# Optimization experiments

Hardware: AMD Instinct MI355X
Metric: run time of the kernel (lower is better)

Reference implementation:

```python
import jax, jax.numpy as jnp
import numpy as np

DIM, WIDTH, POOL, BATCH, SEQ = 4096, 4, 512, 256, 16

def setup_inputs() -> dict:
    key = jax.random.key(0)
    k1, k2, k3, k4 = jax.random.split(key, 4)
    x = jax.random.normal(k1, (BATCH, SEQ, DIM), dtype=jnp.float32)
    conv_state = jax.random.normal(k2, (POOL, WIDTH - 1, DIM), dtype=jnp.float32)
    weight = jax.random.normal(k3, (WIDTH, DIM), dtype=jnp.float32)
    bias = jax.random.normal(k4, (DIM,), dtype=jnp.float32)
    conv_state_indices = jnp.arange(BATCH, dtype=jnp.int32)
    return {"x": x, "conv_state": conv_state, "weight": weight,
            "bias": bias, "conv_state_indices": conv_state_indices}

def reference(x, conv_state, weight, bias, conv_state_indices):
    # x: [b, s, d]; conv_state: [pool, width-1, d]; weight: [width, d]
    b, s, d = x.shape
    width = weight.shape[0]
    state = conv_state[conv_state_indices]            # gather: [b, width-1, d]
    x_new = jnp.concatenate([state, x], axis=1)       # [b, width-1+s, d]
    # depthwise causal conv, width taps (small fixed loop over taps)
    out = bias
    for k in range(width):
        out = out + x_new[:, k:k + s, :] * weight[k]  # [b, s, d]
    out = jax.nn.silu(out)                            # activation=True
    new_state = x_new[:, -(width - 1):, :]            # [b, width-1, d]
    updated_conv_state = conv_state.at[conv_state_indices].set(new_state)
    return out, updated_conv_state
```

## Files before the change

### kernel.cpp

```cpp
#include <hip/hip_runtime.h>

constexpr int DIM   = 4096;
constexpr int WIDTH = 4;
constexpr int POOL  = 512;
constexpr int BATCH = 256;
constexpr int SEQ   = 16;

constexpr int D4_CHUNKS   = DIM / (4 * 256);
constexpr int CONV_BLOCKS = D4_CHUNKS * BATCH;

typedef float f32x4 __attribute__((ext_vector_type(4)));

__device__ __forceinline__ f32x4 ld4(const float* p) {
    return *reinterpret_cast<const f32x4*>(p);
}
__device__ __forceinline__ void st4(float* p, f32x4 v) {
    *reinterpret_cast<f32x4*>(p) = v;
}
__device__ __forceinline__ float fast_silu(float v) {
    return v * __builtin_amdgcn_rcpf(1.0f + __expf(-v));
}

__global__ __launch_bounds__(256, 4) void fused_conv_update_kernel(
    const float* __restrict__ x,
    const float* __restrict__ conv_state,
    const float* __restrict__ weight,
    const float* __restrict__ bias,
    const int*   __restrict__ idxs,
    float*       __restrict__ out,
    float*       __restrict__ out_state)
{
    const int blk   = blockIdx.x;
    const int b     = blk >> 2;
    const int chunk = blk & (D4_CHUNKS - 1);
    const int d     = (chunk * 256 + threadIdx.x) * 4;
    const int idx   = idxs[b];

    const float* xb = x + (size_t)b * SEQ * DIM + d;
    const float* st = conv_state + (size_t)idx * (WIDTH - 1) * DIM + d;

    f32x4 xv[SEQ + WIDTH - 1];
    xv[0] = ld4(st + 0 * DIM);
    xv[1] = ld4(st + 1 * DIM);
    xv[2] = ld4(st + 2 * DIM);
#pragma unroll
    for (int s = 0; s < SEQ; ++s)
        xv[WIDTH - 1 + s] = ld4(xb + (size_t)s * DIM);

    const f32x4 w0 = ld4(weight + 0 * DIM + d);
    const f32x4 w1 = ld4(weight + 1 * DIM + d);
    const f32x4 w2 = ld4(weight + 2 * DIM + d);
    const f32x4 w3 = ld4(weight + 3 * DIM + d);
    const f32x4 bs = ld4(bias + d);

    __builtin_amdgcn_sched_barrier(0);

    float* ob = out + (size_t)b * SEQ * DIM + d;
#pragma unroll
    for (int s = 0; s < SEQ; ++s) {
        f32x4 acc = bs + xv[s] * w0 + xv[s + 1] * w1 + xv[s + 2] * w2 + xv[s + 3] * w3;
        acc.x = fast_silu(acc.x);
        acc.y = fast_silu(acc.y);
        acc.z = fast_silu(acc.z);
        acc.w = fast_silu(acc.w);
        st4(ob + (size_t)s * DIM, acc);
    }

    float* sd = out_state + (size_t)idx * (WIDTH - 1) * DIM + d;
    st4(sd + 0 * DIM, xv[SEQ + 0]);
    st4(sd + 1 * DIM, xv[SEQ + 1]);
    st4(sd + 2 * DIM, xv[SEQ + 2]);

    const int row     = blk >> 1;
    const int halfsel = blk & 1;

    __shared__ int skip;
    if (threadIdx.x == 0) skip = 0;
    __syncthreads();
    if (idxs[threadIdx.x] == row) skip = 1;
    __syncthreads();
    if (skip) return;

    constexpr int HALF_FLOATS = (WIDTH - 1) * DIM / 2;
    const float* src = conv_state + (size_t)row * (WIDTH - 1) * DIM
                     + (size_t)halfsel * HALF_FLOATS;
    float* dst = out_state + (size_t)row * (WIDTH - 1) * DIM
               + (size_t)halfsel * HALF_FLOATS;

    constexpr int HALF_F4 = HALF_FLOATS / 4;
#pragma unroll
    for (int i = threadIdx.x; i < HALF_F4; i += 256)
        st4(dst + (size_t)i * 4, ld4(src + (size_t)i * 4));
}

extern "C" void kernel_launch(void* const* d_in, const int* in_sizes, int n_in,
                              void* d_out, int out_size, void* d_ws, size_t ws_size,
                              hipStream_t stream)
{
    const float* x          = (const float*)d_in[0];
    const float* conv_state = (const float*)d_in[1];
    const float* weight     = (const float*)d_in[2];
    const float* bias       = (const float*)d_in[3];
    const int*   idxs       = (const int*)  d_in[4];

    float* out       = (float*)d_out;
    float* out_state = out + (size_t)BATCH * SEQ * DIM;

    fused_conv_update_kernel<<<CONV_BLOCKS, 256, 0, stream>>>(
        x, conv_state, weight, bias, idxs, out, out_state);
}
```

Measured before the change: 32.53 us.

## Split sequence across two blocks and prefetch pool-copy rows before compute

Each batch/chunk is now split into two blocks covering 8 sequence positions each, doubling the grid to 2048 blocks and halving per-thread register arrays. The second half reloads three overlapping x rows as halo. The untouched-pool-row copy is redistributed into quarter-row slices per block and its loads are issued before the compute. The skip test now uses a per-wave ballot over vectorized index loads instead of shared memory and two __syncthreads. The aim is more parallelism and latency hiding, at the cost of some redundant x reads.

```diff
diff --git a/kernel.cpp b/kernel.cpp
--- a/kernel.cpp
+++ b/kernel.cpp
@@ -6,8 +6,10 @@
 constexpr int BATCH = 256;
 constexpr int SEQ   = 16;
 
+constexpr int S_PER       = 8;
 constexpr int D4_CHUNKS   = DIM / (4 * 256);
-constexpr int CONV_BLOCKS = D4_CHUNKS * BATCH;
+constexpr int BLK_PER_B   = D4_CHUNKS * 2;
+constexpr int CONV_BLOCKS = BLK_PER_B * BATCH;
 
 typedef float f32x4 __attribute__((ext_vector_type(4)));
 
@@ -31,21 +33,29 @@
     float*       __restrict__ out_state)
 {
     const int blk   = blockIdx.x;
-    const int b     = blk >> 2;
-    const int chunk = blk & (D4_CHUNKS - 1);
+    const int b     = blk >> 3;
+    const int rem   = blk & 7;
+    const int chunk = rem >> 1;
+    const int half  = rem & 1;
     const int d     = (chunk * 256 + threadIdx.x) * 4;
     const int idx   = idxs[b];
 
     const float* xb = x + (size_t)b * SEQ * DIM + d;
-    const float* st = conv_state + (size_t)idx * (WIDTH - 1) * DIM + d;
 
-    f32x4 xv[SEQ + WIDTH - 1];
-    xv[0] = ld4(st + 0 * DIM);
-    xv[1] = ld4(st + 1 * DIM);
-    xv[2] = ld4(st + 2 * DIM);
+    f32x4 xv[S_PER + WIDTH - 1];
+    if (half == 0) {
+        const float* st = conv_state + (size_t)idx * (WIDTH - 1) * DIM + d;
+        xv[0] = ld4(st + 0 * DIM);
+        xv[1] = ld4(st + 1 * DIM);
+        xv[2] = ld4(st + 2 * DIM);
 #pragma unroll
-    for (int s = 0; s < SEQ; ++s)
-        xv[WIDTH - 1 + s] = ld4(xb + (size_t)s * DIM);
+        for (int t = 0; t < S_PER; ++t)
+            xv[WIDTH - 1 + t] = ld4(xb + (size_t)t * DIM);
+    } else {
+#pragma unroll
+        for (int t = 0; t < S_PER + WIDTH - 1; ++t)
+            xv[t] = ld4(xb + (size_t)(S_PER - (WIDTH - 1) + t) * DIM);
+    }
 
     const f32x4 w0 = ld4(weight + 0 * DIM + d);
     const f32x4 w1 = ld4(weight + 1 * DIM + d);
@@ -53,11 +63,24 @@
     const f32x4 w3 = ld4(weight + 3 * DIM + d);
     const f32x4 bs = ld4(bias + d);
 
+    const int row = blk >> 2;
+    const int q   = blk & 3;
+    constexpr int Q_FLOATS = (WIDTH - 1) * DIM / 4;
+    const float* csrc = conv_state + (size_t)row * (WIDTH - 1) * DIM
+                      + (size_t)q * Q_FLOATS + threadIdx.x * 4;
+    f32x4 c0 = ld4(csrc + 0 * 1024);
+    f32x4 c1 = ld4(csrc + 1 * 1024);
+    f32x4 c2 = ld4(csrc + 2 * 1024);
+
+    const int4 iv = *reinterpret_cast<const int4*>(idxs + (threadIdx.x & 63) * 4);
+    const bool hit = (iv.x == row) | (iv.y == row) | (iv.z == row) | (iv.w == row);
+    const bool skip = (__ballot(hit) != 0ull);
+
     __builtin_amdgcn_sched_barrier(0);
 
-    float* ob = out + (size_t)b * SEQ * DIM + d;
+    float* ob = out + (size_t)b * SEQ * DIM + (size_t)half * S_PER * DIM + d;
 #pragma unroll
-    for (int s = 0; s < SEQ; ++s) {
+    for (int s = 0; s < S_PER; ++s) {
         f32x4 acc = bs + xv[s] * w0 + xv[s + 1] * w1 + xv[s + 2] * w2 + xv[s + 3] * w3;
         acc.x = fast_silu(acc.x);
         acc.y = fast_silu(acc.y);
@@ -66,31 +89,20 @@
         st4(ob + (size_t)s * DIM, acc);
     }
 
-    float* sd = out_state + (size_t)idx * (WIDTH - 1) * DIM + d;
-    st4(sd + 0 * DIM, xv[SEQ + 0]);
-    st4(sd + 1 * DIM, xv[SEQ + 1]);
-    st4(sd + 2 * DIM, xv[SEQ + 2]);
+    if (half == 1) {
+        float* sd = out_state + (size_t)idx * (WIDTH - 1) * DIM + d;
+        st4(sd + 0 * DIM, xv[S_PER + 0]);
+        st4(sd + 1 * DIM, xv[S_PER + 1]);
+        st4(sd + 2 * DIM, xv[S_PER + 2]);
+    }
 
-    const int row     = blk >> 1;
-    const int halfsel = blk & 1;
-
-    __shared__ int skip;
-    if (threadIdx.x == 0) skip = 0;
-    __syncthreads();
-    if (idxs[threadIdx.x] == row) skip = 1;
-    __syncthreads();
-    if (skip) return;
-
-    constexpr int HALF_FLOATS = (WIDTH - 1) * DIM / 2;
-    const float* src = conv_state + (size_t)row * (WIDTH - 1) * DIM
-                     + (size_t)halfsel * HALF_FLOATS;
-    float* dst = out_state + (size_t)row * (WIDTH - 1) * DIM
-               + (size_t)halfsel * HALF_FLOATS;
-
-    constexpr int HALF_F4 = HALF_FLOATS / 4;
-#pragma unroll
-    for (int i = threadIdx.x; i < HALF_F4; i += 256)
-        st4(dst + (size_t)i * 4, ld4(src + (size_t)i * 4));
+    if (!skip) {
+        float* cdst = out_state + (size_t)row * (WIDTH - 1) * DIM
+                    + (size_t)q * Q_FLOATS + threadIdx.x * 4;
+        st4(cdst + 0 * 1024, c0);
+        st4(cdst + 1 * 1024, c1);
+        st4(cdst + 2 * 1024, c2);
+    }
 }
 
 extern "C" void kernel_launch(void* const* d_in, const int* in_sizes, int n_in,
```

Result: slower. 36.26 us (+11.5%).

## Split work into single-wave blocks with separate conv and state-copy blocks

Applied to the files above, without the earlier changes.

Blocks shrink from 256 to 64 threads, giving 4096 conv blocks, and 4096 extra copy blocks are appended to copy the untouched conv_state rows, so the copy is no longer piggybacked on the conv blocks. The skip check for rows named in the index list now uses a wave ballot over int4-loaded indices instead of shared memory and two __syncthreads. The aim is finer-grained scheduling and the removal of block-level synchronisation. The cost is many more blocks to launch and one idxs scan per copy block.

```diff
diff --git a/kernel.cpp b/kernel.cpp
--- a/kernel.cpp
+++ b/kernel.cpp
@@ -6,8 +6,11 @@
 constexpr int BATCH = 256;
 constexpr int SEQ   = 16;
 
-constexpr int D4_CHUNKS   = DIM / (4 * 256);
-constexpr int CONV_BLOCKS = D4_CHUNKS * BATCH;
+constexpr int WAVES_PER_B  = DIM / (4 * 64);
+constexpr int CONV_BLOCKS  = WAVES_PER_B * BATCH;
+constexpr int COPY_PER_ROW = 8;
+constexpr int COPY_BLOCKS  = COPY_PER_ROW * POOL;
+constexpr int TOTAL_BLOCKS = CONV_BLOCKS + COPY_BLOCKS;
 
 typedef float f32x4 __attribute__((ext_vector_type(4)));
 
@@ -21,7 +24,7 @@
     return v * __builtin_amdgcn_rcpf(1.0f + __expf(-v));
 }
 
-__global__ __launch_bounds__(256, 4) void fused_conv_update_kernel(
+__global__ __launch_bounds__(64) void fused_conv_update_kernel(
     const float* __restrict__ x,
     const float* __restrict__ conv_state,
     const float* __restrict__ weight,
@@ -30,67 +33,75 @@
     float*       __restrict__ out,
     float*       __restrict__ out_state)
 {
-    const int blk   = blockIdx.x;
-    const int b     = blk >> 2;
-    const int chunk = blk & (D4_CHUNKS - 1);
-    const int d     = (chunk * 256 + threadIdx.x) * 4;
-    const int idx   = idxs[b];
+    const int blk  = blockIdx.x;
+    const int lane = threadIdx.x;
 
-    const float* xb = x + (size_t)b * SEQ * DIM + d;
-    const float* st = conv_state + (size_t)idx * (WIDTH - 1) * DIM + d;
+    if (blk < CONV_BLOCKS) {
+        const int b   = blk >> 4;
+        const int wc  = blk & (WAVES_PER_B - 1);
+        const int d   = (wc * 64 + lane) * 4;
+        const int idx = idxs[b];
 
-    f32x4 xv[SEQ + WIDTH - 1];
-    xv[0] = ld4(st + 0 * DIM);
-    xv[1] = ld4(st + 1 * DIM);
-    xv[2] = ld4(st + 2 * DIM);
+        const float* xb = x + (size_t)b * SEQ * DIM + d;
+        const float* st = conv_state + (size_t)idx * (WIDTH - 1) * DIM + d;
+
+        f32x4 xv[SEQ + WIDTH - 1];
+        xv[0] = ld4(st + 0 * DIM);
+        xv[1] = ld4(st + 1 * DIM);
+        xv[2] = ld4(st + 2 * DIM);
 #pragma unroll
-    for (int s = 0; s < SEQ; ++s)
-        xv[WIDTH - 1 + s] = ld4(xb + (size_t)s * DIM);
+        for (int s = 0; s < SEQ; ++s)
+            xv[WIDTH - 1 + s] = ld4(xb + (size_t)s * DIM);
 
-    const f32x4 w0 = ld4(weight + 0 * DIM + d);
-    const f32x4 w1 = ld4(weight + 1 * DIM + d);
-    const f32x4 w2 = ld4(weight + 2 * DIM + d);
-    const f32x4 w3 = ld4(weight + 3 * DIM + d);
-    const f32x4 bs = ld4(bias + d);
+        const f32x4 w0 = ld4(weight + 0 * DIM + d);
+        const f32x4 w1 = ld4(weight + 1 * DIM + d);
+        const f32x4 w2 = ld4(weight + 2 * DIM + d);
+        const f32x4 w3 = ld4(weight + 3 * DIM + d);
+        const f32x4 bs = ld4(bias + d);
 
-    __builtin_amdgcn_sched_barrier(0);
+        float* ob = out + (size_t)b * SEQ * DIM + d;
+#pragma unroll
+        for (int s = 0; s < SEQ; ++s) {
+            f32x4 acc = bs + xv[s] * w0 + xv[s + 1] * w1 + xv[s + 2] * w2 + xv[s + 3] * w3;
+            acc.x = fast_silu(acc.x);
+            acc.y = fast_silu(acc.y);
+            acc.z = fast_silu(acc.z);
+            acc.w = fast_silu(acc.w);
+            st4(ob + (size_t)s * DIM, acc);
+        }
 
-    float* ob = out + (size_t)b * SEQ * DIM + d;
-#pragma unroll
-    for (int s = 0; s < SEQ; ++s) {
-        f32x4 acc = bs + xv[s] * w0 + xv[s + 1] * w1 + xv[s + 2] * w2 + xv[s + 3] * w3;
-        acc.x = fast_silu(acc.x);
-        acc.y = fast_silu(acc.y);
-        acc.z = fast_silu(acc.z);
-        acc.w = fast_silu(acc.w);
-        st4(ob + (size_t)s * DIM, acc);
+        float* sd = out_state + (size_t)idx * (WIDTH - 1) * DIM + d;
+        st4(sd + 0 * DIM, xv[SEQ + 0]);
+        st4(sd + 1 * DIM, xv[SEQ + 1]);
+        st4(sd + 2 * DIM, xv[SEQ + 2]);
+    } else {
+        const int cblk = blk - CONV_BLOCKS;
+        const int row  = cblk >> 3;
+        const int e    = cblk & (COPY_PER_ROW - 1);
+
+        const int4 iv = *reinterpret_cast<const int4*>(idxs + lane * 4);
+        const bool hit = (iv.x == row) | (iv.y == row) | (iv.z == row) | (iv.w == row);
+        if (__ballot(hit) != 0ull) return;
+
+        constexpr int E_FLOATS = (WIDTH - 1) * DIM / COPY_PER_ROW;
+        const float* src = conv_state + (size_t)row * (WIDTH - 1) * DIM
+                         + (size_t)e * E_FLOATS + lane * 4;
+        float* dst = out_state + (size_t)row * (WIDTH - 1) * DIM
+                   + (size_t)e * E_FLOATS + lane * 4;
+
+        f32x4 c0 = ld4(src + 0 * 256);
+        f32x4 c1 = ld4(src + 1 * 256);
+        f32x4 c2 = ld4(src + 2 * 256);
+        f32x4 c3 = ld4(src + 3 * 256);
+        f32x4 c4 = ld4(src + 4 * 256);
+        f32x4 c5 = ld4(src + 5 * 256);
+        st4(dst + 0 * 256, c0);
+        st4(dst + 1 * 256, c1);
+        st4(dst + 2 * 256, c2);
+        st4(dst + 3 * 256, c3);
+        st4(dst + 4 * 256, c4);
+        st4(dst + 5 * 256, c5);
     }
-
-    float* sd = out_state + (size_t)idx * (WIDTH - 1) * DIM + d;
-    st4(sd + 0 * DIM, xv[SEQ + 0]);
-    st4(sd + 1 * DIM, xv[SEQ + 1]);
-    st4(sd + 2 * DIM, xv[SEQ + 2]);
-
-    const int row     = blk >> 1;
-    const int halfsel = blk & 1;
-
-    __shared__ int skip;
-    if (threadIdx.x == 0) skip = 0;
-    __syncthreads();
-    if (idxs[threadIdx.x] == row) skip = 1;
-    __syncthreads();
-    if (skip) return;
-
-    constexpr int HALF_FLOATS = (WIDTH - 1) * DIM / 2;
-    const float* src = conv_state + (size_t)row * (WIDTH - 1) * DIM
-                     + (size_t)halfsel * HALF_FLOATS;
-    float* dst = out_state + (size_t)row * (WIDTH - 1) * DIM
-               + (size_t)halfsel * HALF_FLOATS;
-
-    constexpr int HALF_F4 = HALF_FLOATS / 4;
-#pragma unroll
-    for (int i = threadIdx.x; i < HALF_F4; i += 256)
-        st4(dst + (size_t)i * 4, ld4(src + (size_t)i * 4));
 }
 
 extern "C" void kernel_launch(void* const* d_in, const int* in_sizes, int n_in,
@@ -106,6 +117,6 @@
     float* out       = (float*)d_out;
     float* out_state = out + (size_t)BATCH * SEQ * DIM;
 
-    fused_conv_update_kernel<<<CONV_BLOCKS, 256, 0, stream>>>(
+    fused_conv_update_kernel<<<TOTAL_BLOCKS, 64, 0, stream>>>(
         x, conv_state, weight, bias, idxs, out, out_state);
 }
```

Result: no change. 32.99 us (+1.4%).
